# Kernel tuning notes

Hardware: AMD Instinct MI355X
Metric: run time of the kernel (lower is better)

The kernel has to match this reference:

```python
import jax, jax.numpy as jnp
import numpy as np

H = 2048      # hidden_size
K = 1024      # bottleneck_size
R = 3         # number of roles
B = 8         # batch
S = 2048      # sequence length
LN_EPS = 1e-5


def setup_inputs() -> dict:
    key = jax.random.key(0)
    ks = jax.random.split(key, 8)
    # torch nn.Linear default init ~ U(-1/sqrt(fan_in), 1/sqrt(fan_in)); scale similarly
    sd_d = 1.0 / np.sqrt(H)
    sd_u = 1.0 / np.sqrt(K)
    return {
        "role": jax.random.randint(ks[0], (B,), 0, R),
        "hidden_states": jax.random.normal(ks[1], (B, S, H), dtype=jnp.float32),
        # stacked per-role adapter params
        "W_down": jax.random.uniform(ks[2], (R, H, K), jnp.float32, -sd_d, sd_d),
        "b_down": jax.random.uniform(ks[3], (R, K), jnp.float32, -sd_d, sd_d),
        "W_up": jax.random.uniform(ks[4], (R, K, H), jnp.float32, -sd_u, sd_u),
        "b_up": jax.random.uniform(ks[5], (R, H), jnp.float32, -sd_u, sd_u),
        "gamma": jnp.ones((R, H), jnp.float32),
        "beta": jnp.zeros((R, H), jnp.float32),
    }


def reference(role, hidden_states, W_down, b_down, W_up, b_up, gamma, beta):
    # gather per-sample adapter params by role id: [B, H, K] etc.
    h = jnp.einsum("bsh,bhk->bsk", hidden_states, W_down[role]) + b_down[role][:, None, :]
    h = jax.nn.gelu(h, approximate=False)  # torch nn.GELU default = exact erf
    u = jnp.einsum("bsk,bkh->bsh", h, W_up[role]) + b_up[role][:, None, :]
    y = hidden_states + u
    # LayerNorm over last dim
    mean = jnp.mean(y, axis=-1, keepdims=True)
    var = jnp.mean(jnp.square(y - mean), axis=-1, keepdims=True)
    yn = (y - mean) * jax.lax.rsqrt(var + LN_EPS)
    return yn * gamma[role][:, None, :] + beta[role][:, None, :]
```

## Files before the change

kernel.cpp:

```cpp
#include <hip/hip_runtime.h>
#include <hip/hip_bf16.h>

#define H 2048
#define K 1024
#define R 3
#define BB 8
#define S 2048

typedef __bf16 bf16x8 __attribute__((ext_vector_type(8)));
typedef float f32x4 __attribute__((ext_vector_type(4)));
typedef unsigned short ushort8 __attribute__((ext_vector_type(8)));

static __device__ __forceinline__ unsigned short f2bf(float f) {
    unsigned int u = __float_as_uint(f);
    u += 0x7FFFu + ((u >> 16) & 1u);
    return (unsigned short)(u >> 16);
}

#define GLOAD_LDS16(g, l)                                                      \
    __builtin_amdgcn_global_load_lds(                                          \
        (const __attribute__((address_space(1))) void*)(g),                    \
        (__attribute__((address_space(3))) void*)(l), 16, 0, 0)

__global__ __launch_bounds__(256) void cvt_hs(const float* __restrict__ in,
                                              unsigned short* __restrict__ out,
                                              int n8) {
    int stride = gridDim.x * blockDim.x;
    for (int i = blockIdx.x * blockDim.x + threadIdx.x; i < n8; i += stride) {
        const float4* p = (const float4*)(in + (size_t)i * 8);
        float4 a = p[0], b = p[1];
        union { unsigned short us[8]; ushort8 v; } o;
        o.us[0] = f2bf(a.x); o.us[1] = f2bf(a.y);
        o.us[2] = f2bf(a.z); o.us[3] = f2bf(a.w);
        o.us[4] = f2bf(b.x); o.us[5] = f2bf(b.y);
        o.us[6] = f2bf(b.z); o.us[7] = f2bf(b.w);
        *(ushort8*)(out + (size_t)i * 8) = o.v;
    }
}

__global__ __launch_bounds__(256) void tpose(const float* __restrict__ in,
                                             unsigned short* __restrict__ out,
                                             int rows, int cols) {
    __shared__ float tile[32][33];
    int rr = blockIdx.z;
    const float* ip = in + (size_t)rr * rows * cols;
    unsigned short* op = out + (size_t)rr * rows * cols;
    int x = blockIdx.x * 32 + threadIdx.x;
    int y0 = blockIdx.y * 32 + threadIdx.y;
#pragma unroll
    for (int j = 0; j < 32; j += 8)
        tile[threadIdx.y + j][threadIdx.x] = ip[(size_t)(y0 + j) * cols + x];
    __syncthreads();
    int ox = blockIdx.y * 32 + threadIdx.x;
    int oy0 = blockIdx.x * 32 + threadIdx.y;
#pragma unroll
    for (int j = 0; j < 32; j += 8)
        op[(size_t)(oy0 + j) * rows + ox] = f2bf(tile[threadIdx.x][threadIdx.y + j]);
}

template <int KC, int EPI>
__global__ __launch_bounds__(512, 2) void gemm_8ph(
    const unsigned short* __restrict__ A, const unsigned short* __restrict__ Bt,
    const int* __restrict__ role, const float* __restrict__ bias,
    const unsigned short* __restrict__ resid, void* __restrict__ Out,
    float2* __restrict__ Part, int N) {
    constexpr int NT = KC / 64;
    __shared__ char smem[131072];
    const int tid = threadIdx.x;
    const int wid = tid >> 6, lane = tid & 63;
    const int wm = wid >> 2, wn = wid & 3;
    const int lr = lane & 15, lc = lane >> 4;

    const int nx = N >> 8;
    const int cpx = gridDim.x >> 3;
    const int orig = (blockIdx.x & 7) * cpx + (blockIdx.x >> 3);
    const int tn = orig % nx;
    const int tmz = orig / nx;
    const int tm = tmz & 7;
    const int z = tmz >> 3;
    const int r = role[z];

    const char* Ab = (const char*)(A + ((size_t)z * S + (size_t)tm * 256) * KC);
    const char* Bb = (const char*)(Bt + ((size_t)r * N + (size_t)tn * 256) * KC);

    const int P16 = tid * 16;

#define STAGE16(gbase, ldsoff, kt, half)                                       \
    do {                                                                       \
        _Pragma("unroll") for (int c_ = 0; c_ < 2; c_++) {                     \
            int P_ = c_ * 8192 + P16;                                          \
            int L_ = P_ ^ (((P_ >> 7) & 7) << 4);                              \
            const char* g_ = (gbase) +                                         \
                (size_t)((half) * 128 + (L_ >> 7)) * (KC * 2) +                \
                (size_t)(kt) * 128 + (L_ & 127);                               \
            GLOAD_LDS16(g_, smem + (ldsoff) + (half) * 16384 + P_);            \
        }                                                                      \
    } while (0)

    STAGE16(Ab, 0, 0, 0);        STAGE16(Ab, 0, 0, 1);
    STAGE16(Bb, 32768, 0, 0);    STAGE16(Bb, 32768, 0, 1);
    STAGE16(Bb, 98304, 1, 0);    STAGE16(Bb, 98304, 1, 1);
    asm volatile("s_waitcnt vmcnt(4)" ::: "memory");
    asm volatile("s_barrier" ::: "memory");

    f32x4 acc[8][4] = {};
    const int swz = (lr & 7) << 4;
    const int ck0 = (lc << 4) ^ swz;
    const int ck1 = ck0 ^ 0x40;
    const char* sm = smem;

    bf16x8 aA[4][2], aB[4][2], bL[2][2], bH[2][2];

#define RDA(dst, ibase, SL)                                                    \
    _Pragma("unroll") for (int i_ = 0; i_ < 4; i_++) {                         \
        int rb_ = (wm * 128 + ((ibase) + i_) * 16 + lr) << 7;                  \
        dst[i_][0] = *(const bf16x8*)(sm + (SL) + rb_ + ck0);                  \
        dst[i_][1] = *(const bf16x8*)(sm + (SL) + rb_ + ck1); }
#define RDB(dst, jbase, SL)                                                    \
    _Pragma("unroll") for (int j_ = 0; j_ < 2; j_++) {                         \
        int rb_ = (wn * 64 + ((jbase) + j_) * 16 + lr) << 7;                   \
        dst[j_][0] = *(const bf16x8*)(sm + (SL) + 32768 + rb_ + ck0);          \
        dst[j_][1] = *(const bf16x8*)(sm + (SL) + 32768 + rb_ + ck1); }
#define QMFMA(ar, br, IOFF, JOFF)                                              \
    _Pragma("unroll") for (int kk = 0; kk < 2; kk++)                           \
    _Pragma("unroll") for (int i_ = 0; i_ < 4; i_++)                           \
    _Pragma("unroll") for (int j_ = 0; j_ < 2; j_++)                           \
        acc[(IOFF) + i_][(JOFF) + j_] = __builtin_amdgcn_mfma_f32_16x16x32_bf16( \
            ar[i_][kk], br[j_][kk], acc[(IOFF) + i_][(JOFF) + j_], 0, 0, 0);
#define BAR() asm volatile("s_barrier" ::: "memory")

    RDA(aA, 0, 0);
    RDB(bL, 0, 0);

#pragma unroll 1
    for (int t = 0; t < NT; t += 2) {
        const bool pf = (t + 2) < NT;
        RDB(bH, 2, 0);
        STAGE16(Ab, 65536, t + 1, 0);
        __builtin_amdgcn_s_setprio(1); QMFMA(aA, bL, 0, 0);
        __builtin_amdgcn_s_setprio(0); BAR();
        RDA(aB, 4, 0);
        STAGE16(Ab, 65536, t + 1, 1);
        __builtin_amdgcn_s_setprio(1); QMFMA(aA, bH, 0, 2);
        __builtin_amdgcn_s_setprio(0); BAR();
        if (pf) STAGE16(Bb, 32768, t + 2, 0);
        __builtin_amdgcn_s_setprio(1); QMFMA(aB, bL, 4, 0);
        __builtin_amdgcn_s_setprio(0);
        if (pf) asm volatile("s_waitcnt vmcnt(2)" ::: "memory");
        else    asm volatile("s_waitcnt vmcnt(0)" ::: "memory");
        BAR();
        RDA(aA, 0, 65536);
        RDB(bL, 0, 65536);
        if (pf) STAGE16(Bb, 32768, t + 2, 1);
        __builtin_amdgcn_s_setprio(1); QMFMA(aB, bH, 4, 2);
        __builtin_amdgcn_s_setprio(0); BAR();
        RDB(bH, 2, 65536);
        if (pf) STAGE16(Ab, 0, t + 2, 0);
        __builtin_amdgcn_s_setprio(1); QMFMA(aA, bL, 0, 0);
        __builtin_amdgcn_s_setprio(0); BAR();
        RDA(aB, 4, 65536);
        if (pf) STAGE16(Ab, 0, t + 2, 1);
        __builtin_amdgcn_s_setprio(1); QMFMA(aA, bH, 0, 2);
        __builtin_amdgcn_s_setprio(0); BAR();
        if (pf) STAGE16(Bb, 98304, t + 3, 0);
        __builtin_amdgcn_s_setprio(1); QMFMA(aB, bL, 4, 0);
        __builtin_amdgcn_s_setprio(0);
        if (pf) asm volatile("s_waitcnt vmcnt(2)" ::: "memory");
        BAR();
        if (pf) { RDA(aA, 0, 0); RDB(bL, 0, 0); }
        if (pf) STAGE16(Bb, 98304, t + 3, 1);
        __builtin_amdgcn_s_setprio(1); QMFMA(aB, bH, 4, 2);
        __builtin_amdgcn_s_setprio(0);
        if (pf) BAR();
    }
#undef STAGE16
#undef RDA
#undef RDB
#undef QMFMA
#undef BAR

    const int base_m = tm * 256 + wm * 128;
    const int base_n = tn * 256 + wn * 64;
    float bn[4];
    const float* bp = bias + (size_t)r * N + base_n;
#pragma unroll
    for (int j = 0; j < 4; j++) bn[j] = bp[j * 16 + lr];

    if (EPI == 0) {
        unsigned short* o = (unsigned short*)Out;
#pragma unroll
        for (int i = 0; i < 8; i++) {
#pragma unroll
            for (int j = 0; j < 4; j++) {
#pragma unroll
                for (int q = 0; q < 4; q++) {
                    size_t grow = (size_t)z * S + base_m + i * 16 + lc * 4 + q;
                    int col = base_n + j * 16 + lr;
                    float x = acc[i][j][q] + bn[j];
                    float g = 0.5f * x * (1.0f + erff(x * 0.70710678118654752f));
                    o[grow * N + col] = f2bf(g);
                }
            }
        }
    } else {
        unsigned short* o = (unsigned short*)Out;
        float* pl = (float*)smem;
        __syncthreads();
#pragma unroll
        for (int i = 0; i < 8; i++) {
#pragma unroll
            for (int q = 0; q < 4; q++) {
                size_t grow = (size_t)z * S + base_m + i * 16 + lc * 4 + q;
                float s = 0.f, sq = 0.f;
#pragma unroll
                for (int j = 0; j < 4; j++) {
                    int col = base_n + j * 16 + lr;
                    float rv = __uint_as_float(((unsigned)resid[grow * (size_t)N + col]) << 16);
                    float y = acc[i][j][q] + bn[j] + rv;
                    o[grow * (size_t)N + col] = f2bf(y);
                    s += y; sq += y * y;
                }
#pragma unroll
                for (int off = 1; off < 16; off <<= 1) {
                    s  += __shfl_xor(s, off);
                    sq += __shfl_xor(sq, off);
                }
                if (lr == 0) {
                    int rloc = wm * 128 + i * 16 + lc * 4 + q;
                    pl[wn * 256 + rloc] = s;
                    pl[(4 + wn) * 256 + rloc] = sq;
                }
            }
        }
        __syncthreads();
        if (tid < 256) {
            float s  = pl[tid] + pl[256 + tid] + pl[512 + tid] + pl[768 + tid];
            float sq = pl[1024 + tid] + pl[1280 + tid] + pl[1536 + tid] + pl[1792 + tid];
            size_t grow = (size_t)z * S + tm * 256 + tid;
            Part[(size_t)tn * (BB * S) + grow] = make_float2(s, sq);
        }
    }
}

__global__ __launch_bounds__(256) void ln2(const unsigned short* __restrict__ ybf,
                                           const float2* __restrict__ part,
                                           const int* __restrict__ role,
                                           const float* __restrict__ gamma,
                                           const float* __restrict__ beta,
                                           float* __restrict__ out) {
    int row = blockIdx.x;
    int z = row >> 11;
    int r = role[z];
    float s = 0.f, ss = 0.f;
#pragma unroll
    for (int nb = 0; nb < 8; nb++) {
        float2 p = part[(size_t)nb * (BB * S) + row];
        s += p.x; ss += p.y;
    }
    float mean = s * (1.0f / H);
    float var = ss * (1.0f / H) - mean * mean;
    float rstd = rsqrtf(var + 1e-5f);
    int t = threadIdx.x;
    ushort8 yv = ((const ushort8*)(ybf + (size_t)row * H))[t];
    const float4* gp = (const float4*)(gamma + (size_t)r * H);
    const float4* bp = (const float4*)(beta + (size_t)r * H);
    float4 g0 = gp[2 * t], g1 = gp[2 * t + 1];
    float4 b0 = bp[2 * t], b1 = bp[2 * t + 1];
    float yo[8];
#pragma unroll
    for (int e = 0; e < 8; e++)
        yo[e] = (__uint_as_float(((unsigned)yv[e]) << 16) - mean) * rstd;
    float4 r0, r1;
    r0.x = yo[0] * g0.x + b0.x; r0.y = yo[1] * g0.y + b0.y;
    r0.z = yo[2] * g0.z + b0.z; r0.w = yo[3] * g0.w + b0.w;
    r1.x = yo[4] * g1.x + b1.x; r1.y = yo[5] * g1.y + b1.y;
    r1.z = yo[6] * g1.z + b1.z; r1.w = yo[7] * g1.w + b1.w;
    float4* op = (float4*)(out + (size_t)row * H);
    op[2 * t] = r0;
    op[2 * t + 1] = r1;
}

extern "C" void kernel_launch(void* const* d_in, const int* in_sizes, int n_in,
                              void* d_out, int out_size, void* d_ws, size_t ws_size,
                              hipStream_t stream) {
    const int* role = (const int*)d_in[0];
    const float* hs = (const float*)d_in[1];
    const float* Wd = (const float*)d_in[2];
    const float* bd = (const float*)d_in[3];
    const float* Wu = (const float*)d_in[4];
    const float* bu = (const float*)d_in[5];
    const float* gamma = (const float*)d_in[6];
    const float* beta = (const float*)d_in[7];
    float* out = (float*)d_out;

    char* ws = (char*)d_ws;
    unsigned short* hs_bf = (unsigned short*)ws;
    unsigned short* y_bf = (unsigned short*)ws;
    unsigned short* wd_t = (unsigned short*)(ws + 67108864);
    float2* part = (float2*)(ws + 67108864);
    unsigned short* wu_t = (unsigned short*)(ws + 67108864 + 12582912);
    unsigned short* h_ws = (unsigned short*)(ws + 67108864 + 2 * 12582912);

    cvt_hs<<<4096, 256, 0, stream>>>(hs, hs_bf, (BB * S * H) / 8);
    dim3 tb(32, 8);
    tpose<<<dim3(K / 32, H / 32, R), tb, 0, stream>>>(Wd, wd_t, H, K);
    tpose<<<dim3(H / 32, K / 32, R), tb, 0, stream>>>(Wu, wu_t, K, H);
    gemm_8ph<H, 0><<<(K / 256) * 8 * BB, 512, 0, stream>>>(hs_bf, wd_t, role, bd,
                                                           nullptr, h_ws, nullptr, K);
    gemm_8ph<K, 1><<<(H / 256) * 8 * BB, 512, 0, stream>>>(h_ws, wu_t, role, bu,
                                                           hs_bf, y_bf, part, H);
    ln2<<<BB * S, 256, 0, stream>>>(y_bf, part, role, gamma, beta, out);
}
```

Baseline: 315.2 us.

## Shrink GEMM tile to 256x128 with triple-buffered LDS pipeline

```diff
diff --git a/kernel.cpp b/kernel.cpp
--- a/kernel.cpp
+++ b/kernel.cpp
@@ -59,19 +59,19 @@
 }
 
 template <int KC, int EPI>
-__global__ __launch_bounds__(512, 2) void gemm_8ph(
+__global__ __launch_bounds__(512, 2) void gemm_ra(
     const unsigned short* __restrict__ A, const unsigned short* __restrict__ Bt,
     const int* __restrict__ role, const float* __restrict__ bias,
     const unsigned short* __restrict__ resid, void* __restrict__ Out,
     float2* __restrict__ Part, int N) {
     constexpr int NT = KC / 64;
-    __shared__ char smem[131072];
+    __shared__ char smem[147456];
     const int tid = threadIdx.x;
     const int wid = tid >> 6, lane = tid & 63;
     const int wm = wid >> 2, wn = wid & 3;
     const int lr = lane & 15, lc = lane >> 4;
 
-    const int nx = N >> 8;
+    const int nx = N >> 7;
     const int cpx = gridDim.x >> 3;
     const int orig = (blockIdx.x & 7) * cpx + (blockIdx.x >> 3);
     const int tn = orig % nx;
@@ -81,117 +81,112 @@
     const int r = role[z];
 
     const char* Ab = (const char*)(A + ((size_t)z * S + (size_t)tm * 256) * KC);
-    const char* Bb = (const char*)(Bt + ((size_t)r * N + (size_t)tn * 256) * KC);
+    const char* Bb = (const char*)(Bt + ((size_t)r * N + (size_t)tn * 128) * KC);
 
     const int P16 = tid * 16;
 
-#define STAGE16(gbase, ldsoff, kt, half)                                       \
+#define STGA(sb, kt, c)                                                        \
     do {                                                                       \
-        _Pragma("unroll") for (int c_ = 0; c_ < 2; c_++) {                     \
-            int P_ = c_ * 8192 + P16;                                          \
-            int L_ = P_ ^ (((P_ >> 7) & 7) << 4);                              \
-            const char* g_ = (gbase) +                                         \
-                (size_t)((half) * 128 + (L_ >> 7)) * (KC * 2) +                \
-                (size_t)(kt) * 128 + (L_ & 127);                               \
-            GLOAD_LDS16(g_, smem + (ldsoff) + (half) * 16384 + P_);            \
-        }                                                                      \
+        int P_ = (c) * 8192 + P16;                                             \
+        int L_ = P_ ^ (((P_ >> 7) & 7) << 4);                                  \
+        const char* g_ = Ab + (size_t)(L_ >> 7) * (KC * 2) +                   \
+                         (size_t)(kt) * 128 + (L_ & 127);                      \
+        GLOAD_LDS16(g_, smem + (sb) + P_);                                     \
     } while (0)
-
-    STAGE16(Ab, 0, 0, 0);        STAGE16(Ab, 0, 0, 1);
-    STAGE16(Bb, 32768, 0, 0);    STAGE16(Bb, 32768, 0, 1);
-    STAGE16(Bb, 98304, 1, 0);    STAGE16(Bb, 98304, 1, 1);
-    asm volatile("s_waitcnt vmcnt(4)" ::: "memory");
+#define STGB(sb, kt, c)                                                        \
+    do {                                                                       \
+        int P_ = (c) * 8192 + P16;                                             \
+        int L_ = P_ ^ (((P_ >> 7) & 7) << 4);                                  \
+        const char* g_ = Bb + (size_t)(L_ >> 7) * (KC * 2) +                   \
+                         (size_t)(kt) * 128 + (L_ & 127);                      \
+        GLOAD_LDS16(g_, smem + (sb) + 32768 + P_);                             \
+    } while (0)
+
+    STGA(0, 0, 0); STGA(0, 0, 1); STGA(0, 0, 2); STGA(0, 0, 3);
+    STGB(0, 0, 0); STGB(0, 0, 1);
+    STGA(49152, 1, 0); STGA(49152, 1, 1); STGA(49152, 1, 2); STGA(49152, 1, 3);
+    STGB(49152, 1, 0); STGB(49152, 1, 1);
+    asm volatile("s_waitcnt vmcnt(6)" ::: "memory");
     asm volatile("s_barrier" ::: "memory");
 
-    f32x4 acc[8][4] = {};
+    f32x4 acc[8][2] = {};
     const int swz = (lr & 7) << 4;
     const int ck0 = (lc << 4) ^ swz;
     const int ck1 = ck0 ^ 0x40;
     const char* sm = smem;
 
-    bf16x8 aA[4][2], aB[4][2], bL[2][2], bH[2][2];
-
-#define RDA(dst, ibase, SL)                                                    \
+    bf16x8 A0[4][2], A1[4][2], B0[2][2], B1[2][2];
+
+#define RDA(dst, ih, SB)                                                       \
     _Pragma("unroll") for (int i_ = 0; i_ < 4; i_++) {                         \
-        int rb_ = (wm * 128 + ((ibase) + i_) * 16 + lr) << 7;                  \
-        dst[i_][0] = *(const bf16x8*)(sm + (SL) + rb_ + ck0);                  \
-        dst[i_][1] = *(const bf16x8*)(sm + (SL) + rb_ + ck1); }
-#define RDB(dst, jbase, SL)                                                    \
+        int rb_ = (wm * 128 + ((ih) + i_) * 16 + lr) << 7;                     \
+        dst[i_][0] = *(const bf16x8*)(sm + (SB) + rb_ + ck0);                  \
+        dst[i_][1] = *(const bf16x8*)(sm + (SB) + rb_ + ck1); }
+#define RDB(dst, SB)                                                           \
     _Pragma("unroll") for (int j_ = 0; j_ < 2; j_++) {                         \
-        int rb_ = (wn * 64 + ((jbase) + j_) * 16 + lr) << 7;                   \
-        dst[j_][0] = *(const bf16x8*)(sm + (SL) + 32768 + rb_ + ck0);          \
-        dst[j_][1] = *(const bf16x8*)(sm + (SL) + 32768 + rb_ + ck1); }
-#define QMFMA(ar, br, IOFF, JOFF)                                              \
+        int rb_ = (wn * 32 + j_ * 16 + lr) << 7;                               \
+        dst[j_][0] = *(const bf16x8*)(sm + (SB) + 32768 + rb_ + ck0);          \
+        dst[j_][1] = *(const bf16x8*)(sm + (SB) + 32768 + rb_ + ck1); }
+#define QMFMA(ar, br, IOFF)                                                    \
     _Pragma("unroll") for (int kk = 0; kk < 2; kk++)                           \
     _Pragma("unroll") for (int i_ = 0; i_ < 4; i_++)                           \
     _Pragma("unroll") for (int j_ = 0; j_ < 2; j_++)                           \
-        acc[(IOFF) + i_][(JOFF) + j_] = __builtin_amdgcn_mfma_f32_16x16x32_bf16( \
-            ar[i_][kk], br[j_][kk], acc[(IOFF) + i_][(JOFF) + j_], 0, 0, 0);
+        acc[(IOFF) + i_][j_] = __builtin_amdgcn_mfma_f32_16x16x32_bf16(        \
+            ar[i_][kk], br[j_][kk], acc[(IOFF) + i_][j_], 0, 0, 0);
 #define BAR() asm volatile("s_barrier" ::: "memory")
 
-    RDA(aA, 0, 0);
-    RDB(bL, 0, 0);
-
+    RDA(A0, 0, 0);
+    RDB(B0, 0);
+
+    int s0b = 0, s1b = 49152, s2b = 98304;
 #pragma unroll 1
     for (int t = 0; t < NT; t += 2) {
         const bool pf = (t + 2) < NT;
-        RDB(bH, 2, 0);
-        STAGE16(Ab, 65536, t + 1, 0);
-        __builtin_amdgcn_s_setprio(1); QMFMA(aA, bL, 0, 0);
-        __builtin_amdgcn_s_setprio(0); BAR();
-        RDA(aB, 4, 0);
-        STAGE16(Ab, 65536, t + 1, 1);
-        __builtin_amdgcn_s_setprio(1); QMFMA(aA, bH, 0, 2);
-        __builtin_amdgcn_s_setprio(0); BAR();
-        if (pf) STAGE16(Bb, 32768, t + 2, 0);
-        __builtin_amdgcn_s_setprio(1); QMFMA(aB, bL, 4, 0);
+        RDA(A1, 4, s0b);
+        if (pf) { STGA(s2b, t + 2, 0); STGA(s2b, t + 2, 1); }
+        __builtin_amdgcn_s_setprio(1); QMFMA(A0, B0, 0);
         __builtin_amdgcn_s_setprio(0);
         if (pf) asm volatile("s_waitcnt vmcnt(2)" ::: "memory");
         else    asm volatile("s_waitcnt vmcnt(0)" ::: "memory");
         BAR();
-        RDA(aA, 0, 65536);
-        RDB(bL, 0, 65536);
-        if (pf) STAGE16(Bb, 32768, t + 2, 1);
-        __builtin_amdgcn_s_setprio(1); QMFMA(aB, bH, 4, 2);
+        RDB(B1, s1b); RDA(A0, 0, s1b);
+        if (pf) { STGA(s2b, t + 2, 2); STGA(s2b, t + 2, 3);
+                  STGB(s2b, t + 2, 0); STGB(s2b, t + 2, 1); }
+        __builtin_amdgcn_s_setprio(1); QMFMA(A1, B0, 4);
         __builtin_amdgcn_s_setprio(0); BAR();
-        RDB(bH, 2, 65536);
-        if (pf) STAGE16(Ab, 0, t + 2, 0);
-        __builtin_amdgcn_s_setprio(1); QMFMA(aA, bL, 0, 0);
-        __builtin_amdgcn_s_setprio(0); BAR();
-        RDA(aB, 4, 65536);
-        if (pf) STAGE16(Ab, 0, t + 2, 1);
-        __builtin_amdgcn_s_setprio(1); QMFMA(aA, bH, 0, 2);
-        __builtin_amdgcn_s_setprio(0); BAR();
-        if (pf) STAGE16(Bb, 98304, t + 3, 0);
-        __builtin_amdgcn_s_setprio(1); QMFMA(aB, bL, 4, 0);
+        RDA(A1, 4, s1b);
+        if (pf) { STGA(s0b, t + 3, 0); STGA(s0b, t + 3, 1); }
+        __builtin_amdgcn_s_setprio(1); QMFMA(A0, B1, 0);
         __builtin_amdgcn_s_setprio(0);
         if (pf) asm volatile("s_waitcnt vmcnt(2)" ::: "memory");
         BAR();
-        if (pf) { RDA(aA, 0, 0); RDB(bL, 0, 0); }
-        if (pf) STAGE16(Bb, 98304, t + 3, 1);
-        __builtin_amdgcn_s_setprio(1); QMFMA(aB, bH, 4, 2);
-        __builtin_amdgcn_s_setprio(0);
-        if (pf) BAR();
+        if (pf) { RDB(B0, s2b); RDA(A0, 0, s2b); }
+        if (pf) { STGA(s0b, t + 3, 2); STGA(s0b, t + 3, 3);
+                  STGB(s0b, t + 3, 0); STGB(s0b, t + 3, 1); }
+        __builtin_amdgcn_s_setprio(1); QMFMA(A1, B1, 4);
+        __builtin_amdgcn_s_setprio(0); BAR();
+        int tmp = s0b; s0b = s2b; s2b = s1b; s1b = tmp;
     }
-#undef STAGE16
+#undef STGA
+#undef STGB
 #undef RDA
 #undef RDB
 #undef QMFMA
 #undef BAR
 
     const int base_m = tm * 256 + wm * 128;
-    const int base_n = tn * 256 + wn * 64;
-    float bn[4];
+    const int base_n = tn * 128 + wn * 32;
+    float bn[2];
     const float* bp = bias + (size_t)r * N + base_n;
 #pragma unroll
-    for (int j = 0; j < 4; j++) bn[j] = bp[j * 16 + lr];
+    for (int j = 0; j < 2; j++) bn[j] = bp[j * 16 + lr];
 
     if (EPI == 0) {
         unsigned short* o = (unsigned short*)Out;
 #pragma unroll
         for (int i = 0; i < 8; i++) {
 #pragma unroll
-            for (int j = 0; j < 4; j++) {
+            for (int j = 0; j < 2; j++) {
 #pragma unroll
                 for (int q = 0; q < 4; q++) {
                     size_t grow = (size_t)z * S + base_m + i * 16 + lc * 4 + q;
@@ -213,7 +208,7 @@
                 size_t grow = (size_t)z * S + base_m + i * 16 + lc * 4 + q;
                 float s = 0.f, sq = 0.f;
 #pragma unroll
-                for (int j = 0; j < 4; j++) {
+                for (int j = 0; j < 2; j++) {
                     int col = base_n + j * 16 + lr;
                     float rv = __uint_as_float(((unsigned)resid[grow * (size_t)N + col]) << 16);
                     float y = acc[i][j][q] + bn[j] + rv;
@@ -253,7 +248,7 @@
     int r = role[z];
     float s = 0.f, ss = 0.f;
 #pragma unroll
-    for (int nb = 0; nb < 8; nb++) {
+    for (int nb = 0; nb < 16; nb++) {
         float2 p = part[(size_t)nb * (BB * S) + row];
         s += p.x; ss += p.y;
     }
@@ -305,9 +300,9 @@
     dim3 tb(32, 8);
     tpose<<<dim3(K / 32, H / 32, R), tb, 0, stream>>>(Wd, wd_t, H, K);
     tpose<<<dim3(H / 32, K / 32, R), tb, 0, stream>>>(Wu, wu_t, K, H);
-    gemm_8ph<H, 0><<<(K / 256) * 8 * BB, 512, 0, stream>>>(hs_bf, wd_t, role, bd,
-                                                           nullptr, h_ws, nullptr, K);
-    gemm_8ph<K, 1><<<(H / 256) * 8 * BB, 512, 0, stream>>>(h_ws, wu_t, role, bu,
-                                                           hs_bf, y_bf, part, H);
+    gemm_ra<H, 0><<<(K / 128) * 8 * BB, 512, 0, stream>>>(hs_bf, wd_t, role, bd,
+                                                          nullptr, h_ws, nullptr, K);
+    gemm_ra<K, 1><<<(H / 128) * 8 * BB, 512, 0, stream>>>(h_ws, wu_t, role, bu,
+                                                          hs_bf, y_bf, part, H);
     ln2<<<BB * S, 256, 0, stream>>>(y_bf, part, role, gamma, beta, out);
 }
```

After: 318.2 us. Within noise of the previous version (+0.9%).
